# Optimization experiments

Hardware: AMD Instinct MI355X
Metric: run time of the kernel (lower is better)

## Reference

```python
import jax, jax.numpy as jnp
import numpy as np

N = 4          # BLEU n-gram order
LEN_MAX = 20   # self.len_max
EPS = 1e-9


def _core(tc_res, tc_gts, l_res, l_gts):
    """Clipped n-gram precision pieces for the single hypothesis (r_p_i == 1).
    tc_res: [B, 1, N, K] hypothesis n-gram counts; tc_gts: [B, G, N, K] reference counts;
    l_res: [B, 1], l_gts: [B, G] lengths.
    Returns (g_factor [B,N], und [B,N], l_factor [B])."""
    l_gts = jnp.where(l_gts == 0, LEN_MAX * 10.0, l_gts)            # in-place fixup in torch
    g = tc_res[:, 0]                                                 # [B, N, K]
    l_i = l_res[:, 0]                                                # [B]
    # 'closest' reference-length selection
    idx = jnp.argmin(jnp.abs(l_i[:, None] - l_gts), axis=1)          # [B]
    l_r = jnp.take_along_axis(l_gts, idx[:, None], axis=1)[:, 0]     # [B]
    l_factor = jnp.exp(1.0 - jnp.maximum(1.0 + EPS, (l_r + EPS) / (l_i + EPS)))
    g_gts_max = jnp.max(tc_gts, axis=1)                              # [B, N, K] max over refs
    clipped = jnp.sum(jnp.minimum(g, g_gts_max + EPS), axis=2)       # [B, N]
    # use_bos=True branch: und[:, n] = 1 / (l_i + eps) for every n
    und = jnp.broadcast_to((1.0 / (l_i + EPS))[:, None], clipped.shape)
    return clipped * und, und, l_factor


def reference(tc_res, tc_gts, l_res, l_gts):
    B = tc_res.shape[0]
    g_factor, und, l_factor = _core(tc_res, tc_gts, l_res, l_gts)
    # g_judge: mask of nonzero d(sum g_factor)/d(tc_res) -- the autograd side-channel
    g_judge = jax.grad(lambda t: jnp.sum(_core(t, tc_gts, l_res, l_gts)[0]))(tc_res) != 0
    # 3^N perturbation grid: each n-gram order is {unchanged, +und, relu(-und)}
    ch = jnp.stack([g_factor, g_factor + und, jax.nn.relu(g_factor - und)])   # [3, B, N]
    g_delta = jnp.einsum('ib,jb,kb,lb->bijkl',
                         ch[:, :, 0], ch[:, :, 1], ch[:, :, 2], ch[:, :, 3])  # [B,3,3,3,3]
    flat = g_delta.reshape(B, 3 ** N)
    c_full = l_factor[:, None] * flat ** (1.0 / N)                   # geometric mean * brevity
    c_delta = c_full - c_full[:, -1:]                                # subtract all-minus1 cell
    score_list = c_delta.reshape(B, 1, 3, 3, 3, 3)
    score = c_full[:, 0:1]                                           # c = c_delta_list_[:, 0]
    # score_dif_l: d(loss)/d(l_res); the 3^N block was under torch.no_grad -> detached
    def loss_fn(l_res_):
        gf, _, lf = _core(tc_res, tc_gts, l_res_, l_gts)
        base = jax.lax.stop_gradient(jnp.prod(gf, axis=1))           # == flat[:, 0], detached
        return jnp.sum(lf * base ** (1.0 / N))
    score_dif_l = jax.grad(loss_fn)(l_res)                           # [B, 1]
    return score, score_list, g_judge, score_dif_l


def setup_inputs() -> dict:
    key = jax.random.key(0)
    k1, k2, k3, k4 = jax.random.split(key, 4)
    B, G = 16384, 5
    K = (G + 1) * LEN_MAX + 1  # 121, key_length from process()
    tc_res = jax.random.randint(k1, (B, 1, N, K), 0, 4).astype(jnp.float32)
    tc_gts = jax.random.randint(k2, (B, G, N, K), 0, 4).astype(jnp.float32)
    l_res = jax.random.randint(k3, (B, 1), 1, LEN_MAX + 1).astype(jnp.float32)
    l_gts = jax.random.randint(k4, (B, G), 0, LEN_MAX + 1).astype(jnp.float32)
    return {"tc_res": tc_res, "tc_gts": tc_gts, "l_res": l_res, "l_gts": l_gts}
```

## Files before the change

### kernel.cpp

```cpp
#include <hip/hip_runtime.h>

#define NGRAM 4
#define KDIM 121
#define GDIM 5
#define FEPS 1e-9f
#define NKDIM (NGRAM * KDIM)
#define GNKDIM (GDIM * NKDIM)
#define NCOMBO 81
#define NV4 121

__device__ __forceinline__ float pick3(int s, float x0, float x1, float x2) {
    return (s == 0) ? x0 : ((s == 1) ? x1 : x2);
}

__global__ __launch_bounds__(256) void bleu_kernel(
    const float* __restrict__ tc_res,
    const float* __restrict__ tc_gts,
    const float* __restrict__ l_res,
    const float* __restrict__ l_gts,
    float* __restrict__ o_score,
    float* __restrict__ o_slist,
    float* __restrict__ o_judge,
    float* __restrict__ o_sdl,
    int B)
{
    const int wave = (blockIdx.x * blockDim.x + threadIdx.x) >> 6;
    const int lane = threadIdx.x & 63;
    if (wave >= B) return;
    const int b = wave;

    const float4* __restrict__ res4 = (const float4*)(tc_res + (size_t)b * NKDIM);
    const float4* __restrict__ gts4 = (const float4*)(tc_gts + (size_t)b * GNKDIM);
    float4* __restrict__ judge4 = (float4*)(o_judge + (size_t)b * NKDIM);

    float a0 = 0.0f, a1 = 0.0f, a2 = 0.0f, a3 = 0.0f;

    #pragma unroll
    for (int it = 0; it < 2; ++it) {
        const int vi = it * 64 + lane;
        if (vi < NV4) {
            const float4 g  = res4[vi];
            float4 m        = gts4[0 * NV4 + vi];
            const float4 m1 = gts4[1 * NV4 + vi];
            const float4 m2 = gts4[2 * NV4 + vi];
            const float4 m3 = gts4[3 * NV4 + vi];
            const float4 m4 = gts4[4 * NV4 + vi];
            m.x = fmaxf(fmaxf(fmaxf(m.x, m1.x), fmaxf(m2.x, m3.x)), m4.x);
            m.y = fmaxf(fmaxf(fmaxf(m.y, m1.y), fmaxf(m2.y, m3.y)), m4.y);
            m.z = fmaxf(fmaxf(fmaxf(m.z, m1.z), fmaxf(m2.z, m3.z)), m4.z);
            m.w = fmaxf(fmaxf(fmaxf(m.w, m1.w), fmaxf(m2.w, m3.w)), m4.w);
            const float mx = m.x + FEPS, my = m.y + FEPS,
                        mz = m.z + FEPS, mw = m.w + FEPS;

            float4 j;
            j.x = (g.x <= mx) ? 1.0f : 0.0f;
            j.y = (g.y <= my) ? 1.0f : 0.0f;
            j.z = (g.z <= mz) ? 1.0f : 0.0f;
            j.w = (g.w <= mw) ? 1.0f : 0.0f;
            judge4[vi] = j;

            const float cx = fminf(g.x, mx);
            const float cy = fminf(g.y, my);
            const float cz = fminf(g.z, mz);
            const float cw = fminf(g.w, mw);

            const int idx = vi * 4;
            const int n0 = (idx >= KDIM) + (idx >= 2 * KDIM) + (idx >= 3 * KDIM);
            const int n3 = (idx + 3 >= KDIM) + (idx + 3 >= 2 * KDIM) + (idx + 3 >= 3 * KDIM);
            if (n0 == n3) {
                const float s = (cx + cy) + (cz + cw);
                a0 += (n0 == 0) ? s : 0.0f;
                a1 += (n0 == 1) ? s : 0.0f;
                a2 += (n0 == 2) ? s : 0.0f;
                a3 += (n0 == 3) ? s : 0.0f;
            } else {
                const float ce[4] = { cx, cy, cz, cw };
                #pragma unroll
                for (int e = 0; e < 4; ++e) {
                    const int ie = idx + e;
                    const int ne = (ie >= KDIM) + (ie >= 2 * KDIM) + (ie >= 3 * KDIM);
                    const float v = ce[e];
                    a0 += (ne == 0) ? v : 0.0f;
                    a1 += (ne == 1) ? v : 0.0f;
                    a2 += (ne == 2) ? v : 0.0f;
                    a3 += (ne == 3) ? v : 0.0f;
                }
            }
        }
    }

    #pragma unroll
    for (int s = 1; s < 64; s <<= 1) {
        a0 += __shfl_xor(a0, s, 64);
        a1 += __shfl_xor(a1, s, 64);
        a2 += __shfl_xor(a2, s, 64);
        a3 += __shfl_xor(a3, s, 64);
    }

    const float l_i = l_res[b];
    float best_d = 1e30f;
    float l_r = 0.0f;
    #pragma unroll
    for (int g = 0; g < GDIM; ++g) {
        float lg = l_gts[(size_t)b * GDIM + g];
        lg = (lg == 0.0f) ? 200.0f : lg;
        const float d = fabsf(l_i - lg);
        if (d < best_d) { best_d = d; l_r = lg; }
    }

    const float li_e = l_i + FEPS;
    const float und = 1.0f / li_e;
    const float r = (l_r + FEPS) / li_e;
    const float lf = expf(1.0f - fmaxf(1.0f, r));

    const float gf0 = a0 * und;
    const float gf1 = a1 * und;
    const float gf2 = a2 * und;
    const float gf3 = a3 * und;

    const float c00 = gf0, c01 = gf1, c02 = gf2, c03 = gf3;
    const float c10 = gf0 + und, c11 = gf1 + und, c12 = gf2 + und, c13 = gf3 + und;
    const float c20 = fmaxf(gf0 - und, 0.0f);
    const float c21 = fmaxf(gf1 - und, 0.0f);
    const float c22 = fmaxf(gf2 - und, 0.0f);
    const float c23 = fmaxf(gf3 - und, 0.0f);

    const float p_last = c20 * c21 * c22 * c23;
    const float cf_last = lf * sqrtf(sqrtf(p_last));

    for (int c = lane; c < NCOMBO; c += 64) {
        const int i = c / 27;
        const int j = (c / 9) % 3;
        const int kk = (c / 3) % 3;
        const int l = c % 3;
        const float p = pick3(i, c00, c10, c20) *
                        pick3(j, c01, c11, c21) *
                        pick3(kk, c02, c12, c22) *
                        pick3(l, c03, c13, c23);
        const float cf = lf * sqrtf(sqrtf(p));
        o_slist[(size_t)b * NCOMBO + c] = cf - cf_last;
        if (c == 0) o_score[b] = cf;
    }

    if (lane == 0) {
        const float base = gf0 * gf1 * gf2 * gf3;
        const float w = (r > 1.0f) ? 1.0f : ((r == 1.0f) ? 0.5f : 0.0f);
        o_sdl[b] = sqrtf(sqrtf(base)) * lf * w * (l_r + FEPS) / (li_e * li_e);
    }
}

extern "C" void kernel_launch(void* const* d_in, const int* in_sizes, int n_in,
                              void* d_out, int out_size, void* d_ws, size_t ws_size,
                              hipStream_t stream) {
    const float* tc_res = (const float*)d_in[0];
    const float* tc_gts = (const float*)d_in[1];
    const float* l_res  = (const float*)d_in[2];
    const float* l_gts  = (const float*)d_in[3];
    const int B = in_sizes[2];

    float* out = (float*)d_out;
    float* o_score = out;
    float* o_slist = o_score + B;
    float* o_judge = o_slist + (size_t)B * NCOMBO;
    float* o_sdl   = o_judge + (size_t)B * NKDIM;

    const int waves_per_block = 4;
    const int blocks = (B + waves_per_block - 1) / waves_per_block;
    bleu_kernel<<<blocks, 256, 0, stream>>>(tc_res, tc_gts, l_res, l_gts,
                                            o_score, o_slist, o_judge, o_sdl, B);
}
```

Before: 41.31 us.

## Assign two waves per batch row with LDS cross-wave reduction

Each batch row is now handled by 128 threads (two waves) instead of one wave looping twice, so each thread loads a single float4 slice and the loop disappears. Per-wave partial sums are combined through shared memory after a block-wide sync. The launch-bounds hint also requests higher occupancy. In exchange the kernel launches twice as many waves, each with less work, and adds a barrier plus extra reduction traffic.

```diff
diff --git a/kernel.cpp b/kernel.cpp
--- a/kernel.cpp
+++ b/kernel.cpp
@@ -13,7 +13,7 @@
     return (s == 0) ? x0 : ((s == 1) ? x1 : x2);
 }
 
-__global__ __launch_bounds__(256) void bleu_kernel(
+__global__ __launch_bounds__(256, 8) void bleu_kernel(
     const float* __restrict__ tc_res,
     const float* __restrict__ tc_gts,
     const float* __restrict__ l_res,
@@ -24,67 +24,65 @@
     float* __restrict__ o_sdl,
     int B)
 {
-    const int wave = (blockIdx.x * blockDim.x + threadIdx.x) >> 6;
-    const int lane = threadIdx.x & 63;
-    if (wave >= B) return;
-    const int b = wave;
-
-    const float4* __restrict__ res4 = (const float4*)(tc_res + (size_t)b * NKDIM);
-    const float4* __restrict__ gts4 = (const float4*)(tc_gts + (size_t)b * GNKDIM);
-    float4* __restrict__ judge4 = (float4*)(o_judge + (size_t)b * NKDIM);
+    const int tid  = threadIdx.x;
+    const int half = tid >> 7;
+    const int t2   = tid & 127;
+    const int lane = tid & 63;
+    const int wv   = (tid >> 6) & 1;
+    const int b    = blockIdx.x * 2 + half;
+    const bool valid = (b < B);
 
     float a0 = 0.0f, a1 = 0.0f, a2 = 0.0f, a3 = 0.0f;
 
-    #pragma unroll
-    for (int it = 0; it < 2; ++it) {
-        const int vi = it * 64 + lane;
-        if (vi < NV4) {
-            const float4 g  = res4[vi];
-            float4 m        = gts4[0 * NV4 + vi];
-            const float4 m1 = gts4[1 * NV4 + vi];
-            const float4 m2 = gts4[2 * NV4 + vi];
-            const float4 m3 = gts4[3 * NV4 + vi];
-            const float4 m4 = gts4[4 * NV4 + vi];
-            m.x = fmaxf(fmaxf(fmaxf(m.x, m1.x), fmaxf(m2.x, m3.x)), m4.x);
-            m.y = fmaxf(fmaxf(fmaxf(m.y, m1.y), fmaxf(m2.y, m3.y)), m4.y);
-            m.z = fmaxf(fmaxf(fmaxf(m.z, m1.z), fmaxf(m2.z, m3.z)), m4.z);
-            m.w = fmaxf(fmaxf(fmaxf(m.w, m1.w), fmaxf(m2.w, m3.w)), m4.w);
-            const float mx = m.x + FEPS, my = m.y + FEPS,
-                        mz = m.z + FEPS, mw = m.w + FEPS;
+    if (valid && t2 < NV4) {
+        const float4* __restrict__ res4 = (const float4*)(tc_res + (size_t)b * NKDIM);
+        const float4* __restrict__ gts4 = (const float4*)(tc_gts + (size_t)b * GNKDIM);
+        const int vi = t2;
 
-            float4 j;
-            j.x = (g.x <= mx) ? 1.0f : 0.0f;
-            j.y = (g.y <= my) ? 1.0f : 0.0f;
-            j.z = (g.z <= mz) ? 1.0f : 0.0f;
-            j.w = (g.w <= mw) ? 1.0f : 0.0f;
-            judge4[vi] = j;
+        const float4 g  = res4[vi];
+        const float4 m0 = gts4[0 * NV4 + vi];
+        const float4 m1 = gts4[1 * NV4 + vi];
+        const float4 m2 = gts4[2 * NV4 + vi];
+        const float4 m3 = gts4[3 * NV4 + vi];
+        const float4 m4 = gts4[4 * NV4 + vi];
 
-            const float cx = fminf(g.x, mx);
-            const float cy = fminf(g.y, my);
-            const float cz = fminf(g.z, mz);
-            const float cw = fminf(g.w, mw);
+        const float mx = fmaxf(fmaxf(fmaxf(m0.x, m1.x), fmaxf(m2.x, m3.x)), m4.x) + FEPS;
+        const float my = fmaxf(fmaxf(fmaxf(m0.y, m1.y), fmaxf(m2.y, m3.y)), m4.y) + FEPS;
+        const float mz = fmaxf(fmaxf(fmaxf(m0.z, m1.z), fmaxf(m2.z, m3.z)), m4.z) + FEPS;
+        const float mw = fmaxf(fmaxf(fmaxf(m0.w, m1.w), fmaxf(m2.w, m3.w)), m4.w) + FEPS;
 
-            const int idx = vi * 4;
-            const int n0 = (idx >= KDIM) + (idx >= 2 * KDIM) + (idx >= 3 * KDIM);
-            const int n3 = (idx + 3 >= KDIM) + (idx + 3 >= 2 * KDIM) + (idx + 3 >= 3 * KDIM);
-            if (n0 == n3) {
-                const float s = (cx + cy) + (cz + cw);
-                a0 += (n0 == 0) ? s : 0.0f;
-                a1 += (n0 == 1) ? s : 0.0f;
-                a2 += (n0 == 2) ? s : 0.0f;
-                a3 += (n0 == 3) ? s : 0.0f;
-            } else {
-                const float ce[4] = { cx, cy, cz, cw };
-                #pragma unroll
-                for (int e = 0; e < 4; ++e) {
-                    const int ie = idx + e;
-                    const int ne = (ie >= KDIM) + (ie >= 2 * KDIM) + (ie >= 3 * KDIM);
-                    const float v = ce[e];
-                    a0 += (ne == 0) ? v : 0.0f;
-                    a1 += (ne == 1) ? v : 0.0f;
-                    a2 += (ne == 2) ? v : 0.0f;
-                    a3 += (ne == 3) ? v : 0.0f;
-                }
+        float4 j;
+        j.x = (g.x <= mx) ? 1.0f : 0.0f;
+        j.y = (g.y <= my) ? 1.0f : 0.0f;
+        j.z = (g.z <= mz) ? 1.0f : 0.0f;
+        j.w = (g.w <= mw) ? 1.0f : 0.0f;
+        ((float4*)(o_judge + (size_t)b * NKDIM))[vi] = j;
+
+        const float cx = fminf(g.x, mx);
+        const float cy = fminf(g.y, my);
+        const float cz = fminf(g.z, mz);
+        const float cw = fminf(g.w, mw);
+
+        const int idx = vi * 4;
+        const int n0 = (idx >= KDIM) + (idx >= 2 * KDIM) + (idx >= 3 * KDIM);
+        const int n3 = (idx + 3 >= KDIM) + (idx + 3 >= 2 * KDIM) + (idx + 3 >= 3 * KDIM);
+        if (n0 == n3) {
+            const float s = (cx + cy) + (cz + cw);
+            a0 += (n0 == 0) ? s : 0.0f;
+            a1 += (n0 == 1) ? s : 0.0f;
+            a2 += (n0 == 2) ? s : 0.0f;
+            a3 += (n0 == 3) ? s : 0.0f;
+        } else {
+            const float ce[4] = { cx, cy, cz, cw };
+            #pragma unroll
+            for (int e = 0; e < 4; ++e) {
+                const int ie = idx + e;
+                const int ne = (ie >= KDIM) + (ie >= 2 * KDIM) + (ie >= 3 * KDIM);
+                const float v = ce[e];
+                a0 += (ne == 0) ? v : 0.0f;
+                a1 += (ne == 1) ? v : 0.0f;
+                a2 += (ne == 2) ? v : 0.0f;
+                a3 += (ne == 3) ? v : 0.0f;
             }
         }
     }
@@ -96,6 +94,18 @@
         a2 += __shfl_xor(a2, s, 64);
         a3 += __shfl_xor(a3, s, 64);
     }
+
+    __shared__ float4 red[2][2];
+    if (lane == 0) red[half][wv] = make_float4(a0, a1, a2, a3);
+    __syncthreads();
+    const float4 r0 = red[half][0];
+    const float4 r1 = red[half][1];
+    const float s0 = r0.x + r1.x;
+    const float s1 = r0.y + r1.y;
+    const float s2 = r0.z + r1.z;
+    const float s3 = r0.w + r1.w;
+
+    if (!valid) return;
 
     const float l_i = l_res[b];
     float best_d = 1e30f;
@@ -113,10 +123,10 @@
     const float r = (l_r + FEPS) / li_e;
     const float lf = expf(1.0f - fmaxf(1.0f, r));
 
-    const float gf0 = a0 * und;
-    const float gf1 = a1 * und;
-    const float gf2 = a2 * und;
-    const float gf3 = a3 * und;
+    const float gf0 = s0 * und;
+    const float gf1 = s1 * und;
+    const float gf2 = s2 * und;
+    const float gf3 = s3 * und;
 
     const float c00 = gf0, c01 = gf1, c02 = gf2, c03 = gf3;
     const float c10 = gf0 + und, c11 = gf1 + und, c12 = gf2 + und, c13 = gf3 + und;
@@ -128,7 +138,8 @@
     const float p_last = c20 * c21 * c22 * c23;
     const float cf_last = lf * sqrtf(sqrtf(p_last));
 
-    for (int c = lane; c < NCOMBO; c += 64) {
+    if (t2 < NCOMBO) {
+        const int c = t2;
         const int i = c / 27;
         const int j = (c / 9) % 3;
         const int kk = (c / 3) % 3;
@@ -139,13 +150,12 @@
                         pick3(l, c03, c13, c23);
         const float cf = lf * sqrtf(sqrtf(p));
         o_slist[(size_t)b * NCOMBO + c] = cf - cf_last;
-        if (c == 0) o_score[b] = cf;
-    }
-
-    if (lane == 0) {
-        const float base = gf0 * gf1 * gf2 * gf3;
-        const float w = (r > 1.0f) ? 1.0f : ((r == 1.0f) ? 0.5f : 0.0f);
-        o_sdl[b] = sqrtf(sqrtf(base)) * lf * w * (l_r + FEPS) / (li_e * li_e);
+        if (c == 0) {
+            o_score[b] = cf;
+            const float base = gf0 * gf1 * gf2 * gf3;
+            const float w = (r > 1.0f) ? 1.0f : ((r == 1.0f) ? 0.5f : 0.0f);
+            o_sdl[b] = sqrtf(sqrtf(base)) * lf * w * (l_r + FEPS) / (li_e * li_e);
+        }
     }
 }
 
@@ -164,8 +174,7 @@
     float* o_judge = o_slist + (size_t)B * NCOMBO;
     float* o_sdl   = o_judge + (size_t)B * NKDIM;
 
-    const int waves_per_block = 4;
-    const int blocks = (B + waves_per_block - 1) / waves_per_block;
+    const int blocks = (B + 1) / 2;
     bleu_kernel<<<blocks, 256, 0, stream>>>(tc_res, tc_gts, l_res, l_gts,
                                             o_score, o_slist, o_judge, o_sdl, B);
 }
```

Result: no change. 41.32 us (+0.0%).
